# Kernel tuning notes

Measured on AMD Instinct MI355X. Metric: run time of the kernel, lower is better.

The kernel has to match this reference:

```python
import jax, jax.numpy as jnp
import numpy as np

LN_EPS = 1e-5

def _reduce(t, ln_gamma, ln_beta, w_red, b_red):
    # LayerNorm(dim) then Linear(dim -> 16)
    mu = jnp.mean(t, axis=-1, keepdims=True)
    var = jnp.mean((t - mu) ** 2, axis=-1, keepdims=True)
    t = (t - mu) / jnp.sqrt(var + LN_EPS) * ln_gamma + ln_beta
    return t @ w_red + b_red  # [b, s, 16]

def setup_inputs() -> dict:
    key = jax.random.key(0)
    ks = jax.random.split(key, 4)
    b, m, n, dim, pair_dim = 1, 512, 512, 384, 128
    x = jax.random.normal(ks[0], (b, m, dim), dtype=jnp.float32)
    y = jax.random.normal(ks[1], (b, n, dim), dtype=jnp.float32)
    w_red = jax.random.normal(ks[2], (dim, 16), dtype=jnp.float32) / np.sqrt(dim)
    b_red = jnp.zeros((16,), dtype=jnp.float32)
    w_out = jax.random.normal(ks[3], (16 * 16, pair_dim), dtype=jnp.float32) / 16.0
    b_out = jnp.zeros((pair_dim,), dtype=jnp.float32)
    ln_gamma = jnp.ones((dim,), dtype=jnp.float32)
    ln_beta = jnp.zeros((dim,), dtype=jnp.float32)
    return {"x": x, "y": y, "ln_gamma": ln_gamma, "ln_beta": ln_beta,
            "w_red": w_red, "b_red": b_red, "w_out": w_out, "b_out": b_out}

def reference(x, y, ln_gamma, ln_beta, w_red, b_red, w_out, b_out):
    xr = _reduce(x, ln_gamma, ln_beta, w_red, b_red)  # [b, m, 16]
    yr = _reduce(y, ln_gamma, ln_beta, w_red, b_red)  # [b, n, 16]
    # outer product: [b, m, n, 16, 16]
    outer = jnp.einsum('bmi,bnj->bmnij', xr, yr)
    b_, m_, n_ = outer.shape[:3]
    outer = outer.reshape(b_, m_, n_, 16 * 16)
    return outer @ w_out + b_out  # [b, m, n, pair_dim]
```

## Files before the change

### kernel.cpp

```cpp
#include <hip/hip_runtime.h>

#define DIM 384
#define RD  16
#define PD  128
#define MTILE 256
#define LN_EPS 1e-5f

__global__ __launch_bounds__(128) void ln_reduce_kernel(
    const float* __restrict__ x, const float* __restrict__ y,
    const float* __restrict__ gamma, const float* __restrict__ beta,
    const float* __restrict__ w_red, const float* __restrict__ b_red,
    float* __restrict__ xr, float* __restrict__ yr, int M)
{
  int row = blockIdx.x;
  const float* src;
  float* dst;
  if (row < M) { src = x + (size_t)row * DIM;       dst = xr + (size_t)row * RD; }
  else         { src = y + (size_t)(row - M) * DIM; dst = yr + (size_t)(row - M) * RD; }

  int t = threadIdx.x;
  float v[3];
#pragma unroll
  for (int k = 0; k < 3; ++k) v[k] = src[t + k * 128];

  __shared__ float red[2];
  __shared__ float nrm[DIM];

  float s = v[0] + v[1] + v[2];
#pragma unroll
  for (int off = 32; off; off >>= 1) s += __shfl_down(s, off);
  int wave = t >> 6, lane = t & 63;
  if (lane == 0) red[wave] = s;
  __syncthreads();
  float mu = (red[0] + red[1]) * (1.0f / DIM);
  __syncthreads();

  float d0 = v[0] - mu, d1 = v[1] - mu, d2 = v[2] - mu;
  float s2 = d0 * d0 + d1 * d1 + d2 * d2;
#pragma unroll
  for (int off = 32; off; off >>= 1) s2 += __shfl_down(s2, off);
  if (lane == 0) red[wave] = s2;
  __syncthreads();
  float var = (red[0] + red[1]) * (1.0f / DIM);
  float rsig = rsqrtf(var + LN_EPS);

#pragma unroll
  for (int k = 0; k < 3; ++k) {
    int d = t + k * 128;
    nrm[d] = (v[k] - mu) * rsig * gamma[d] + beta[d];
  }
  __syncthreads();

  int j  = t >> 3;
  int k0 = t & 7;
  float p = 0.f;
  for (int e = k0; e < DIM; e += 8)
    p += nrm[e] * w_red[e * RD + j];
  p += __shfl_xor(p, 1);
  p += __shfl_xor(p, 2);
  p += __shfl_xor(p, 4);
  if (k0 == 0) dst[j] = p + b_red[j];
}

__global__ __launch_bounds__(256) void opm_kernel(
    const float* __restrict__ xr, const float* __restrict__ yr,
    const float* __restrict__ w_out, const float* __restrict__ b_out,
    float* __restrict__ out, int Nn)
{
  __shared__ float Wn[RD][PD];
  __shared__ float xs[MTILE][RD];
  __shared__ float yn[RD];

  int n  = blockIdx.y;
  int m0 = blockIdx.x * MTILE;
  int t  = threadIdx.x;

  if (t < RD) yn[t] = yr[n * RD + t];

  {
    float4* xsf = (float4*)&xs[0][0];
    const float4* xrf = (const float4*)(xr + (size_t)m0 * RD);
#pragma unroll
    for (int k = 0; k < 4; ++k) xsf[t + k * 256] = xrf[t + k * 256];
  }
  __syncthreads();

  {
    int p  = t & 127;
    int i0 = (t >> 7) * 8;
#pragma unroll
    for (int k = 0; k < 8; ++k) {
      int i = i0 + k;
      float acc = 0.f;
#pragma unroll
      for (int j = 0; j < RD; ++j)
        acc += yn[j] * w_out[(size_t)(i * RD + j) * PD + p];
      Wn[i][p] = acc;
    }
  }
  __syncthreads();

  int p4 = (t & 31) * 4;
  int g  = t >> 5;

  float4 w[RD];
#pragma unroll
  for (int i = 0; i < RD; ++i) w[i] = *(const float4*)&Wn[i][p4];
  float4 bo = *(const float4*)&b_out[p4];

  for (int mi = g; mi < MTILE; mi += 8) {
    float xv[RD];
#pragma unroll
    for (int k = 0; k < 4; ++k)
      *(float4*)&xv[k * 4] = *(const float4*)&xs[mi][k * 4];

    float4 acc = bo;
#pragma unroll
    for (int i = 0; i < RD; ++i) {
      acc.x += xv[i] * w[i].x;
      acc.y += xv[i] * w[i].y;
      acc.z += xv[i] * w[i].z;
      acc.w += xv[i] * w[i].w;
    }
    size_t m = (size_t)(m0 + mi);
    *(float4*)&out[(m * Nn + n) * PD + p4] = acc;
  }
}

extern "C" void kernel_launch(void* const* d_in, const int* in_sizes, int n_in,
                              void* d_out, int out_size, void* d_ws, size_t ws_size,
                              hipStream_t stream) {
  const float* x        = (const float*)d_in[0];
  const float* y        = (const float*)d_in[1];
  const float* ln_gamma = (const float*)d_in[2];
  const float* ln_beta  = (const float*)d_in[3];
  const float* w_red    = (const float*)d_in[4];
  const float* b_red    = (const float*)d_in[5];
  const float* w_out    = (const float*)d_in[6];
  const float* b_out    = (const float*)d_in[7];
  float* out = (float*)d_out;

  int M = in_sizes[0] / DIM;
  int N = in_sizes[1] / DIM;

  float* xr = (float*)d_ws;
  float* yr = xr + (size_t)M * RD;

  ln_reduce_kernel<<<M + N, 128, 0, stream>>>(x, y, ln_gamma, ln_beta,
                                              w_red, b_red, xr, yr, M);

  dim3 grid(M / MTILE, N);
  opm_kernel<<<grid, 256, 0, stream>>>(xr, yr, w_out, b_out, out, N);
}
```

Baseline: 47.14 us.

## Fold xr into w_out per row m and stream contiguous output rows

The output kernel now gives each block one m row. It folds xr[m] into w_out to form a per-row 16x128 matrix, loads all of yr into shared memory, and loops over n, writing contiguous output rows with nontemporal stores. Before, each block handled one n and a 256-row m tile, so its output writes were strided by N*PD. The change is meant to make writes contiguous and cut the number of small blocks. In exchange it uses 32KB of shared memory per block, hardcodes NN=512 for the shared buffer size, and launches only 512 blocks.

```diff
diff --git a/kernel.cpp b/kernel.cpp
--- a/kernel.cpp
+++ b/kernel.cpp
@@ -3,8 +3,10 @@
 #define DIM 384
 #define RD  16
 #define PD  128
-#define MTILE 256
+#define NN  512
 #define LN_EPS 1e-5f
+
+typedef float fx4 __attribute__((ext_vector_type(4)));
 
 __global__ __launch_bounds__(128) void ln_reduce_kernel(
     const float* __restrict__ x, const float* __restrict__ y,
@@ -62,40 +64,39 @@
   if (k0 == 0) dst[j] = p + b_red[j];
 }
 
-__global__ __launch_bounds__(256) void opm_kernel(
+__global__ __launch_bounds__(512) void opm_kernel(
     const float* __restrict__ xr, const float* __restrict__ yr,
     const float* __restrict__ w_out, const float* __restrict__ b_out,
-    float* __restrict__ out, int Nn)
+    float* __restrict__ out, int N)
 {
-  __shared__ float Wn[RD][PD];
-  __shared__ float xs[MTILE][RD];
-  __shared__ float yn[RD];
+  __shared__ float Vm[RD][PD];
+  __shared__ float yrs[NN * RD];
+  __shared__ float xm[RD];
 
-  int n  = blockIdx.y;
-  int m0 = blockIdx.x * MTILE;
-  int t  = threadIdx.x;
+  int m = blockIdx.x;
+  int t = threadIdx.x;
 
-  if (t < RD) yn[t] = yr[n * RD + t];
+  if (t < RD) xm[t] = xr[(size_t)m * RD + t];
 
   {
-    float4* xsf = (float4*)&xs[0][0];
-    const float4* xrf = (const float4*)(xr + (size_t)m0 * RD);
-#pragma unroll
-    for (int k = 0; k < 4; ++k) xsf[t + k * 256] = xrf[t + k * 256];
+    fx4* d = (fx4*)yrs;
+    const fx4* s4 = (const fx4*)yr;
+    int total = N * RD / 4;
+    for (int idx = t; idx < total; idx += 512) d[idx] = s4[idx];
   }
   __syncthreads();
 
   {
     int p  = t & 127;
-    int i0 = (t >> 7) * 8;
+    int j0 = (t >> 7) * 4;
 #pragma unroll
-    for (int k = 0; k < 8; ++k) {
-      int i = i0 + k;
+    for (int jj = 0; jj < 4; ++jj) {
+      int j = j0 + jj;
       float acc = 0.f;
 #pragma unroll
-      for (int j = 0; j < RD; ++j)
-        acc += yn[j] * w_out[(size_t)(i * RD + j) * PD + p];
-      Wn[i][p] = acc;
+      for (int i = 0; i < RD; ++i)
+        acc += xm[i] * w_out[(size_t)(i * RD + j) * PD + p];
+      Vm[j][p] = acc;
     }
   }
   __syncthreads();
@@ -103,27 +104,25 @@
   int p4 = (t & 31) * 4;
   int g  = t >> 5;
 
-  float4 w[RD];
+  fx4 w[RD];
 #pragma unroll
-  for (int i = 0; i < RD; ++i) w[i] = *(const float4*)&Wn[i][p4];
-  float4 bo = *(const float4*)&b_out[p4];
+  for (int j = 0; j < RD; ++j) w[j] = *(const fx4*)&Vm[j][p4];
+  fx4 bo = *(const fx4*)&b_out[p4];
 
-  for (int mi = g; mi < MTILE; mi += 8) {
-    float xv[RD];
+  float* obase = out + (size_t)m * N * PD + p4;
+
+#pragma unroll 2
+  for (int n = g; n < N; n += 16) {
+    float yv[RD];
 #pragma unroll
     for (int k = 0; k < 4; ++k)
-      *(float4*)&xv[k * 4] = *(const float4*)&xs[mi][k * 4];
+      *(fx4*)&yv[k * 4] = *(const fx4*)&yrs[n * RD + k * 4];
 
-    float4 acc = bo;
+    fx4 acc = bo;
 #pragma unroll
-    for (int i = 0; i < RD; ++i) {
-      acc.x += xv[i] * w[i].x;
-      acc.y += xv[i] * w[i].y;
-      acc.z += xv[i] * w[i].z;
-      acc.w += xv[i] * w[i].w;
-    }
-    size_t m = (size_t)(m0 + mi);
-    *(float4*)&out[(m * Nn + n) * PD + p4] = acc;
+    for (int j = 0; j < RD; ++j)
+      acc += yv[j] * w[j];
+    __builtin_nontemporal_store(acc, (fx4*)(obase + (size_t)n * PD));
   }
 }
 
@@ -149,6 +148,5 @@
   ln_reduce_kernel<<<M + N, 128, 0, stream>>>(x, y, ln_gamma, ln_beta,
                                               w_red, b_red, xr, yr, M);
 
-  dim3 grid(M / MTILE, N);
-  opm_kernel<<<grid, 256, 0, stream>>>(xr, yr, w_out, b_out, out, N);
+  opm_kernel<<<M, 512, 0, stream>>>(xr, yr, w_out, b_out, out, N);
 }
```

Result: faster. 44.76 us (-5.0%).
